# Kernel optimization log

Measured on AMD Instinct MI355X. Metric: run time of the kernel, lower is better.

## Reference

```python
import jax, jax.numpy as jnp
import numpy as np

E, H, F, T = 8, 2048, 4096, 16384  # experts, hidden, ffn, total tokens


def setup_inputs() -> dict:
    key = jax.random.key(0)
    k1, k2, k3 = jax.random.split(key, 3)
    std = 1.0 / np.sqrt(H)
    x = jax.random.normal(k1, (T, H), dtype=jnp.float32)
    # trunc_normal_(std=std) ~ normal * std for reference purposes
    w_gate_up = jax.random.normal(k2, (E, 2 * F, H), dtype=jnp.float32) * std
    w_down = jax.random.normal(k3, (E, H, F), dtype=jnp.float32) * std
    # tokens are pre-sorted by expert; uniform routing: T//E tokens per expert
    tokens_per_expert = jnp.full((E,), T // E, dtype=jnp.int64)
    return {"x": x, "w_gate_up": w_gate_up, "w_down": w_down,
            "tokens_per_expert": tokens_per_expert}


def reference(x, w_gate_up, w_down, tokens_per_expert):
    # x: [T, H] sorted by expert; uniform tokens_per_expert => grouped GEMM
    # is a batched GEMM over the expert axis (same math as the per-expert
    # sequential fallback: gate_up = xi @ w_gate_up[i].T, etc.).
    e = w_gate_up.shape[0]
    f = w_down.shape[2]
    xe = x.reshape(e, -1, x.shape[-1])                     # [E, T/E, H]
    gate_up = jnp.einsum('eth,efh->etf', xe, w_gate_up)    # [E, T/E, 2F]
    gate, up = gate_up[..., :f], gate_up[..., f:]
    hidden = jax.nn.silu(gate) * up                        # [E, T/E, F]
    out = jnp.einsum('etf,ehf->eth', hidden, w_down)       # [E, T/E, H]
    return out.reshape(x.shape)
```

## Files before the change

### kernel.cpp

```cpp
#include <hip/hip_runtime.h>
#include <stdint.h>

typedef unsigned short u16;
typedef unsigned int u32;
typedef short bf16x8 __attribute__((ext_vector_type(8)));
typedef float f32x4 __attribute__((ext_vector_type(4)));

#define E_ 8
#define H_ 2048
#define F_ 4096
#define T_ 16384
#define TE_ 2048

#define WAITV(n) asm volatile("s_waitcnt vmcnt(" #n ")" ::: "memory")
#define FENCE asm volatile("" ::: "memory")
#define BAR __builtin_amdgcn_s_barrier()

__device__ __forceinline__ u16 f2bf(float f) {
  u32 u = __builtin_bit_cast(u32, f);
  u32 r = (u + 0x7FFFu + ((u >> 16) & 1u)) >> 16;
  return (u16)r;
}

__device__ __forceinline__ void gload16(const u16* g, u16* l) {
  __builtin_amdgcn_global_load_lds(
      (__attribute__((address_space(1))) void*)g,
      (__attribute__((address_space(3))) void*)l, 16, 0, 0);
}

__device__ __forceinline__ void mfma_b(f32x4& acc, bf16x8 a, bf16x8 b) {
  asm volatile("v_mfma_f32_16x16x32_bf16 %0, %1, %2, %0"
               : "+v"(acc)
               : "v"(a), "v"(b));
}


__global__ __launch_bounds__(256) void cvt_kernel(const float* __restrict__ src,
                                                  u16* __restrict__ dst,
                                                  long n4) {
  long i = (long)blockIdx.x * blockDim.x + threadIdx.x;
  long stride = (long)gridDim.x * blockDim.x;
  const float4* s4 = (const float4*)src;
  uint2* d4 = (uint2*)dst;
  for (; i < n4; i += stride) {
    float4 v = s4[i];
    uint2 o;
    o.x = (u32)f2bf(v.x) | ((u32)f2bf(v.y) << 16);
    o.y = (u32)f2bf(v.z) | ((u32)f2bf(v.w) << 16);
    d4[i] = o;
  }
}


__global__ __launch_bounds__(512) void gemm1_silu(const u16* __restrict__ Xb,
                                                  const u16* __restrict__ Wgu,
                                                  u16* __restrict__ Hid,
                                                  long sX, long sW, long sH) {
  const int z = blockIdx.z;
  Xb += (long)z * sX;
  Wgu += (long)z * sW;
  Hid += (long)z * sH;

  const int bx = blockIdx.x;
  const int by = blockIdx.y;
  const int tid = threadIdx.x;
  const int w = tid >> 6;
  const int lane = tid & 63;
  const int wr = w >> 2, wc = w & 3;

  __shared__ __attribute__((aligned(16))) u16 lds[3 * 24576];

  const int srow = (w << 3) + (lane >> 3);
  const int scol = (((lane & 7) ^ (lane >> 3)) << 3);
  const u16* gA = Xb + (size_t)((by << 7) + srow) * H_ + scol;
  const u16* gBg = Wgu + (size_t)((bx << 7) + srow) * H_ + scol;
  const u16* gBu = gBg + (size_t)F_ * H_;

  auto stage = [&](int t, int buf) {
    u16* L = &lds[buf * 24576];
    const int ko = t << 6;
    const int wb = w << 3;
#pragma unroll
    for (int i = 0; i < 2; ++i) {
      gload16(gA + (size_t)(i * 64) * H_ + ko, &L[((i << 6) + wb) << 6]);
      gload16(gBg + (size_t)(i * 64) * H_ + ko,
              &L[8192 + (((i << 6) + wb) << 6)]);
      gload16(gBu + (size_t)(i * 64) * H_ + ko,
              &L[16384 + (((i << 6) + wb) << 6)]);
    }
  };

  f32x4 accG[4][2] = {};
  f32x4 accU[4][2] = {};
  const int fr = lane & 15, q = lane >> 4, l7 = lane & 7;

  auto comp = [&](int buf) {
    const u16* L = &lds[buf * 24576];
    bf16x8 a[4][2], bg[2][2], bu[2][2];
#pragma unroll
    for (int ni = 0; ni < 2; ++ni)
#pragma unroll
      for (int ks = 0; ks < 2; ++ks) {
        int r = (wc << 5) + (ni << 4) + fr;
        int off = (r << 6) + ((((ks << 2) + q) ^ l7) << 3);
        bg[ni][ks] = *(const bf16x8*)&L[8192 + off];
        bu[ni][ks] = *(const bf16x8*)&L[16384 + off];
      }
#pragma unroll
    for (int mi = 0; mi < 4; ++mi)
#pragma unroll
      for (int ks = 0; ks < 2; ++ks) {
        int r = (wr << 6) + (mi << 4) + fr;
        a[mi][ks] = *(const bf16x8*)&L[(r << 6) + ((((ks << 2) + q) ^ l7) << 3)];
      }
    __builtin_amdgcn_s_setprio(1);
#pragma unroll
    for (int mi = 0; mi < 4; ++mi)
#pragma unroll
      for (int ni = 0; ni < 2; ++ni)
#pragma unroll
        for (int ks = 0; ks < 2; ++ks) {
          mfma_b(accG[mi][ni], a[mi][ks], bg[ni][ks]);
          mfma_b(accU[mi][ni], a[mi][ks], bu[ni][ks]);
        }
    __builtin_amdgcn_s_setprio(0);
  };

  const int NT = H_ / 64;
  stage(0, 0);
  stage(1, 1);
  int b0 = 0, b1 = 1, b2 = 2;
  for (int t = 0; t < NT - 2; ++t) {
    stage(t + 2, b2);
    WAITV(12);
    BAR;
    FENCE;
    comp(b0);
    FENCE;
    BAR;
    int tmp = b0; b0 = b1; b1 = b2; b2 = tmp;
  }
  WAITV(6); BAR; FENCE;
  comp(b0);
  FENCE; BAR;
  WAITV(0); BAR; FENCE;
  comp(b1);

  const int row0 = (by << 7) + (wr << 6) + (q << 2);
  const int col0 = (bx << 7) + (wc << 5) + fr;
#pragma unroll
  for (int mi = 0; mi < 4; ++mi)
#pragma unroll
    for (int ni = 0; ni < 2; ++ni)
#pragma unroll
      for (int j = 0; j < 4; ++j) {
        float g = accG[mi][ni][j];
        float u = accU[mi][ni][j];
        float h = (g / (1.f + __expf(-g))) * u;
        Hid[(size_t)(row0 + (mi << 4) + j) * F_ + col0 + (ni << 4)] = f2bf(h);
      }
}


__global__ __launch_bounds__(512) void gemm2_down(const u16* __restrict__ Hd,
                                                  const u16* __restrict__ Wd,
                                                  float* __restrict__ Out,
                                                  long sH, long sW, long sO) {
  const int z = blockIdx.z;
  Hd += (long)z * sH;
  Wd += (long)z * sW;
  Out += (long)z * sO;

  const int bx = blockIdx.x;
  const int by = blockIdx.y;
  const int tid = threadIdx.x;
  const int w = tid >> 6;
  const int lane = tid & 63;
  const int wr = w >> 1, wc = w & 1;

  __shared__ __attribute__((aligned(16))) u16 lds[3 * 24576];

  const int srow = (w << 3) + (lane >> 3);
  const int scol = (((lane & 7) ^ (lane >> 3)) << 3);
  const u16* gA = Hd + (size_t)((by << 8) + srow) * F_ + scol;
  const u16* gB = Wd + (size_t)((bx << 7) + srow) * F_ + scol;

  auto stage = [&](int t, int buf) {
    u16* L = &lds[buf * 24576];
    const int ko = t << 6;
    const int wb = w << 3;
#pragma unroll
    for (int i = 0; i < 4; ++i)
      gload16(gA + (size_t)(i * 64) * F_ + ko, &L[((i << 6) + wb) << 6]);
#pragma unroll
    for (int i = 0; i < 2; ++i)
      gload16(gB + (size_t)(i * 64) * F_ + ko,
              &L[16384 + (((i << 6) + wb) << 6)]);
  };

  f32x4 acc[4][4] = {};
  const int fr = lane & 15, q = lane >> 4, l7 = lane & 7;

  auto comp = [&](int buf) {
    const u16* L = &lds[buf * 24576];
    bf16x8 a[4][2], b[4][2];
#pragma unroll
    for (int ni = 0; ni < 4; ++ni)
#pragma unroll
      for (int ks = 0; ks < 2; ++ks) {
        int r = (wc << 6) + (ni << 4) + fr;
        b[ni][ks] =
            *(const bf16x8*)&L[16384 + (r << 6) + ((((ks << 2) + q) ^ l7) << 3)];
      }
#pragma unroll
    for (int mi = 0; mi < 4; ++mi)
#pragma unroll
      for (int ks = 0; ks < 2; ++ks) {
        int r = (wr << 6) + (mi << 4) + fr;
        a[mi][ks] = *(const bf16x8*)&L[(r << 6) + ((((ks << 2) + q) ^ l7) << 3)];
      }
    __builtin_amdgcn_s_setprio(1);
#pragma unroll
    for (int mi = 0; mi < 4; ++mi)
#pragma unroll
      for (int ni = 0; ni < 4; ++ni)
#pragma unroll
        for (int ks = 0; ks < 2; ++ks)
          mfma_b(acc[mi][ni], a[mi][ks], b[ni][ks]);
    __builtin_amdgcn_s_setprio(0);
  };

  const int NT = F_ / 64;
  stage(0, 0);
  stage(1, 1);
  int b0 = 0, b1 = 1, b2 = 2;
  for (int t = 0; t < NT - 2; ++t) {
    stage(t + 2, b2);
    WAITV(12);
    BAR;
    FENCE;
    comp(b0);
    FENCE;
    BAR;
    int tmp = b0; b0 = b1; b1 = b2; b2 = tmp;
  }
  WAITV(6); BAR; FENCE;
  comp(b0);
  FENCE; BAR;
  WAITV(0); BAR; FENCE;
  comp(b1);

  const int row0 = (by << 8) + (wr << 6) + (q << 2);
  const int col0 = (bx << 7) + (wc << 6) + fr;
#pragma unroll
  for (int mi = 0; mi < 4; ++mi)
#pragma unroll
    for (int ni = 0; ni < 4; ++ni)
#pragma unroll
      for (int j = 0; j < 4; ++j)
        Out[(size_t)(row0 + (mi << 4) + j) * H_ + col0 + (ni << 4)] =
            acc[mi][ni][j];
}


extern "C" void kernel_launch(void* const* d_in, const int* in_sizes, int n_in,
                              void* d_out, int out_size, void* d_ws,
                              size_t ws_size, hipStream_t stream) {
  (void)in_sizes;
  (void)n_in;
  (void)out_size;
  const float* x = (const float*)d_in[0];
  const float* wgu = (const float*)d_in[1];
  const float* wdn = (const float*)d_in[2];
  float* out = (float*)d_out;
  u16* ws = (u16*)d_ws;

  const size_t xbN = (size_t)T_ * H_;
  const size_t wguN = (size_t)E_ * 2 * F_ * H_;
  const size_t wdnN = (size_t)E_ * H_ * F_;
  const size_t hidN = (size_t)T_ * F_;
  const size_t fullBytes = (xbN + wguN + wdnN + hidN) * 2;

  dim3 cblk(256), gblk(512);

  if (ws_size >= fullBytes) {
    u16* xb = ws;
    u16* wgub = xb + xbN;
    u16* wdnb = wgub + wguN;
    u16* hid = wdnb + wdnN;
    cvt_kernel<<<2048, cblk, 0, stream>>>(x, xb, (long)(xbN / 4));
    cvt_kernel<<<4096, cblk, 0, stream>>>(wgu, wgub, (long)(wguN / 4));
    cvt_kernel<<<4096, cblk, 0, stream>>>(wdn, wdnb, (long)(wdnN / 4));
    gemm1_silu<<<dim3(F_ / 128, TE_ / 128, E_), gblk, 0, stream>>>(
        xb, wgub, hid, (long)TE_ * H_, (long)2 * F_ * H_, (long)TE_ * F_);
    gemm2_down<<<dim3(H_ / 128, TE_ / 256, E_), gblk, 0, stream>>>(
        hid, wdnb, out, (long)TE_ * F_, (long)H_ * F_, (long)TE_ * H_);
  } else {
    u16* xb = ws;
    u16* wgub = xb + (size_t)TE_ * H_;
    u16* wdnb = wgub + (size_t)2 * F_ * H_;
    u16* hid = wdnb + (size_t)H_ * F_;
    for (int e = 0; e < E_; ++e) {
      cvt_kernel<<<1024, cblk, 0, stream>>>(x + (size_t)e * TE_ * H_, xb,
                                            (long)((size_t)TE_ * H_ / 4));
      cvt_kernel<<<2048, cblk, 0, stream>>>(wgu + (size_t)e * 2 * F_ * H_, wgub,
                                            (long)((size_t)2 * F_ * H_ / 4));
      cvt_kernel<<<2048, cblk, 0, stream>>>(wdn + (size_t)e * H_ * F_, wdnb,
                                            (long)((size_t)H_ * F_ / 4));
      gemm1_silu<<<dim3(F_ / 128, TE_ / 128, 1), gblk, 0, stream>>>(xb, wgub,
                                                                    hid, 0, 0,
                                                                    0);
      gemm2_down<<<dim3(H_ / 128, TE_ / 256, 1), gblk, 0, stream>>>(
          hid, wdnb, out + (size_t)e * TE_ * H_, 0, 0, 0);
    }
  }
}
```

Measured before the change: 1.126 ms.

## Rewrite both GEMMs with 256x256 tiles, finer-grained pipelined LDS staging and XCD swizzle

Both GEMM kernels move to 256x256 output tiles per workgroup (gate and up interleaved within the B tile for gemm1). K-chunks are split into half-steps whose loads, LDS reads and MFMA bursts are interleaved with barriers in a double-buffered schedule. Block indices are remapped across chiplets for better L2 locality, and launch bounds ask for 2 waves per SIMD. The goal is higher arithmetic intensity per byte loaded and less stalling on memory. In exchange the kernel holds many more accumulator registers, and the new LDS layout has no XOR swizzle, which may cause bank conflicts.

After: 1.214 ms. +7.8%, slower.

```diff
diff --git a/kernel.cpp b/kernel.cpp
--- a/kernel.cpp
+++ b/kernel.cpp
@@ -13,8 +13,12 @@
 #define TE_ 2048
 
 #define WAITV(n) asm volatile("s_waitcnt vmcnt(" #n ")" ::: "memory")
-#define FENCE asm volatile("" ::: "memory")
-#define BAR __builtin_amdgcn_s_barrier()
+#define BARF                              \
+  do {                                    \
+    asm volatile("" ::: "memory");        \
+    __builtin_amdgcn_s_barrier();         \
+    asm volatile("" ::: "memory");        \
+  } while (0)
 
 __device__ __forceinline__ u16 f2bf(float f) {
   u32 u = __builtin_bit_cast(u32, f);
@@ -52,214 +56,219 @@
 }
 
 
-__global__ __launch_bounds__(512) void gemm1_silu(const u16* __restrict__ Xb,
-                                                  const u16* __restrict__ Wgu,
-                                                  u16* __restrict__ Hid,
-                                                  long sX, long sW, long sH) {
-  const int z = blockIdx.z;
-  Xb += (long)z * sX;
-  Wgu += (long)z * sW;
-  Hid += (long)z * sH;
-
-  const int bx = blockIdx.x;
-  const int by = blockIdx.y;
-  const int tid = threadIdx.x;
-  const int w = tid >> 6;
-  const int lane = tid & 63;
+__global__ __launch_bounds__(512, 2) void gemm1_silu(
+    const u16* __restrict__ Xb, const u16* __restrict__ Wgu,
+    u16* __restrict__ Hid) {
+  const int nx = gridDim.x, ny = gridDim.y;
+  int lin = blockIdx.x + nx * (blockIdx.y + ny * blockIdx.z);
+  const int nwg = nx * ny * gridDim.z;
+  int swz = (lin & 7) * (nwg >> 3) + (lin >> 3);
+  const int bx = swz % nx;
+  int tq = swz / nx;
+  const int by = tq % ny;
+  const int z = tq / ny;
+  Xb += (size_t)z * TE_ * H_;
+  Wgu += (size_t)z * 2 * F_ * H_;
+  Hid += (size_t)z * TE_ * F_;
+
+  const int tid = threadIdx.x, w = tid >> 6, lane = tid & 63;
   const int wr = w >> 2, wc = w & 3;
-
-  __shared__ __attribute__((aligned(16))) u16 lds[3 * 24576];
-
-  const int srow = (w << 3) + (lane >> 3);
-  const int scol = (((lane & 7) ^ (lane >> 3)) << 3);
-  const u16* gA = Xb + (size_t)((by << 7) + srow) * H_ + scol;
-  const u16* gBg = Wgu + (size_t)((bx << 7) + srow) * H_ + scol;
-  const u16* gBu = gBg + (size_t)F_ * H_;
-
-  auto stage = [&](int t, int buf) {
-    u16* L = &lds[buf * 24576];
-    const int ko = t << 6;
-    const int wb = w << 3;
+  const int r15 = lane & 15, g4 = lane >> 4;
+
+  __shared__ __attribute__((aligned(16))) u16 lds[65536];
+
+  const u16* gA = Xb + (size_t)(by * 256 + r15) * H_ + g4 * 8;
+  const u16* gB =
+      Wgu + (size_t)(((w & 1) ? F_ : 0) + bx * 128 + r15) * H_ + g4 * 8;
+
+  auto stA = [&](int t, int kh, int buf) {
 #pragma unroll
     for (int i = 0; i < 2; ++i) {
-      gload16(gA + (size_t)(i * 64) * H_ + ko, &L[((i << 6) + wb) << 6]);
-      gload16(gBg + (size_t)(i * 64) * H_ + ko,
-              &L[8192 + (((i << 6) + wb) << 6)]);
-      gload16(gBu + (size_t)(i * 64) * H_ + ko,
-              &L[16384 + (((i << 6) + wb) << 6)]);
-    }
-  };
-
-  f32x4 accG[4][2] = {};
-  f32x4 accU[4][2] = {};
-  const int fr = lane & 15, q = lane >> 4, l7 = lane & 7;
-
-  auto comp = [&](int buf) {
-    const u16* L = &lds[buf * 24576];
-    bf16x8 a[4][2], bg[2][2], bu[2][2];
-#pragma unroll
-    for (int ni = 0; ni < 2; ++ni)
-#pragma unroll
-      for (int ks = 0; ks < 2; ++ks) {
-        int r = (wc << 5) + (ni << 4) + fr;
-        int off = (r << 6) + ((((ks << 2) + q) ^ l7) << 3);
-        bg[ni][ks] = *(const bf16x8*)&L[8192 + off];
-        bu[ni][ks] = *(const bf16x8*)&L[16384 + off];
+      const int c = i * 8 + w;
+      gload16(gA + (size_t)(c * 16) * H_ + t * 64 + kh * 32,
+              lds + buf * 32768 + kh * 8192 + c * 512);
+    }
+  };
+  auto stB = [&](int t, int kh, int buf) {
+#pragma unroll
+    for (int i = 0; i < 2; ++i) {
+      const int c = i * 8 + w;
+      gload16(gB + (size_t)((i * 4 + (w >> 1)) * 16) * H_ + t * 64 + kh * 32,
+              lds + buf * 32768 + 16384 + kh * 8192 + c * 512);
+    }
+  };
+
+  const u16* ldsA = lds + lane * 8;
+  const u16* ldsB = lds + 16384 + lane * 8;
+
+  f32x4 acc[8][4] = {};
+  bf16x8 a[4], b[4];
+
+  auto dsB = [&](int buf, int kh) {
+#pragma unroll
+    for (int ni = 0; ni < 4; ++ni)
+      b[ni] =
+          *(const bf16x8*)&ldsB[buf * 32768 + kh * 8192 + (wc * 4 + ni) * 512];
+  };
+  auto dsA = [&](int buf, int kh, int mh) {
+#pragma unroll
+    for (int mi = 0; mi < 4; ++mi)
+      a[mi] = *(const bf16x8*)&ldsA[buf * 32768 + kh * 8192 +
+                                    (wr * 8 + mh * 4 + mi) * 512];
+  };
+  auto mm = [&](int mh) {
+    __builtin_amdgcn_s_setprio(1);
+#pragma unroll
+    for (int mi = 0; mi < 4; ++mi)
+#pragma unroll
+      for (int ni = 0; ni < 4; ++ni) mfma_b(acc[mh * 4 + mi][ni], a[mi], b[ni]);
+    __builtin_amdgcn_s_setprio(0);
+  };
+
+  stB(0, 0, 0); stA(0, 0, 0); stB(0, 1, 0); stA(0, 1, 0);
+  stB(1, 0, 1); stA(1, 0, 1); stB(1, 1, 1);
+  WAITV(6);
+  BARF;
+
+  const int NT = H_ / 64;
+  for (int t = 0; t <= NT - 4; t += 2) {
+    dsB(0, 0); dsA(0, 0, 0); stA(t + 1, 1, 1);           BARF; mm(0); BARF;
+    dsA(0, 0, 1);            stB(t + 2, 0, 0);           BARF; mm(1); BARF;
+    dsB(0, 1); dsA(0, 1, 0); stA(t + 2, 0, 0);           BARF; mm(0); BARF;
+    dsA(0, 1, 1);            stB(t + 2, 1, 0); WAITV(6); BARF; mm(1); BARF;
+    dsB(1, 0); dsA(1, 0, 0); stA(t + 2, 1, 0);           BARF; mm(0); BARF;
+    dsA(1, 0, 1);            stB(t + 3, 0, 1);           BARF; mm(1); BARF;
+    dsB(1, 1); dsA(1, 1, 0); stA(t + 3, 0, 1);           BARF; mm(0); BARF;
+    dsA(1, 1, 1);            stB(t + 3, 1, 1); WAITV(6); BARF; mm(1); BARF;
+  }
+  dsB(0, 0); dsA(0, 0, 0); stA(NT - 1, 1, 1); BARF; mm(0); BARF;
+  dsA(0, 0, 1);                               BARF; mm(1); BARF;
+  dsB(0, 1); dsA(0, 1, 0);                    BARF; mm(0); BARF;
+  dsA(0, 1, 1);            WAITV(0);          BARF; mm(1); BARF;
+  dsB(1, 0); dsA(1, 0, 0);                    BARF; mm(0); BARF;
+  dsA(1, 0, 1);                               BARF; mm(1); BARF;
+  dsB(1, 1); dsA(1, 1, 0);                    BARF; mm(0); BARF;
+  dsA(1, 1, 1);                               BARF; mm(1);
+
+  const int row0 = by * 256 + wr * 128 + g4 * 4;
+  const int colb = bx * 128 + wc * 32 + r15;
+#pragma unroll
+  for (int mI = 0; mI < 8; ++mI)
+#pragma unroll
+    for (int k = 0; k < 2; ++k)
+#pragma unroll
+      for (int j = 0; j < 4; ++j) {
+        float g = acc[mI][2 * k][j];
+        float u = acc[mI][2 * k + 1][j];
+        float h = (g / (1.f + __expf(-g))) * u;
+        Hid[(size_t)(row0 + mI * 16 + j) * F_ + colb + k * 16] = f2bf(h);
       }
+}
+
+
+__global__ __launch_bounds__(512, 2) void gemm2_down(
+    const u16* __restrict__ Hd, const u16* __restrict__ Wd,
+    float* __restrict__ Out) {
+  const int nx = gridDim.x, ny = gridDim.y;
+  int lin = blockIdx.x + nx * (blockIdx.y + ny * blockIdx.z);
+  const int nwg = nx * ny * gridDim.z;
+  int swz = (lin & 7) * (nwg >> 3) + (lin >> 3);
+  const int bx = swz % nx;
+  int tq = swz / nx;
+  const int by = tq % ny;
+  const int z = tq / ny;
+  Hd += (size_t)z * TE_ * F_;
+  Wd += (size_t)z * H_ * F_;
+  Out += (size_t)z * TE_ * H_;
+
+  const int tid = threadIdx.x, w = tid >> 6, lane = tid & 63;
+  const int wr = w >> 2, wc = w & 3;
+  const int r15 = lane & 15, g4 = lane >> 4;
+
+  __shared__ __attribute__((aligned(16))) u16 lds[65536];
+
+  const u16* gA = Hd + (size_t)(by * 256 + r15) * F_ + g4 * 8;
+  const u16* gB = Wd + (size_t)(bx * 256 + r15) * F_ + g4 * 8;
+
+  auto stA = [&](int t, int kh, int buf) {
+#pragma unroll
+    for (int i = 0; i < 2; ++i) {
+      const int c = i * 8 + w;
+      gload16(gA + (size_t)(c * 16) * F_ + t * 64 + kh * 32,
+              lds + buf * 32768 + kh * 8192 + c * 512);
+    }
+  };
+  auto stB = [&](int t, int kh, int buf) {
+#pragma unroll
+    for (int i = 0; i < 2; ++i) {
+      const int c = i * 8 + w;
+      gload16(gB + (size_t)(c * 16) * F_ + t * 64 + kh * 32,
+              lds + buf * 32768 + 16384 + kh * 8192 + c * 512);
+    }
+  };
+
+  const u16* ldsA = lds + lane * 8;
+  const u16* ldsB = lds + 16384 + lane * 8;
+
+  f32x4 acc[8][4] = {};
+  bf16x8 a[4], b[4];
+
+  auto dsB = [&](int buf, int kh) {
+#pragma unroll
+    for (int ni = 0; ni < 4; ++ni)
+      b[ni] =
+          *(const bf16x8*)&ldsB[buf * 32768 + kh * 8192 + (wc * 4 + ni) * 512];
+  };
+  auto dsA = [&](int buf, int kh, int mh) {
 #pragma unroll
     for (int mi = 0; mi < 4; ++mi)
-#pragma unroll
-      for (int ks = 0; ks < 2; ++ks) {
-        int r = (wr << 6) + (mi << 4) + fr;
-        a[mi][ks] = *(const bf16x8*)&L[(r << 6) + ((((ks << 2) + q) ^ l7) << 3)];
-      }
+      a[mi] = *(const bf16x8*)&ldsA[buf * 32768 + kh * 8192 +
+                                    (wr * 8 + mh * 4 + mi) * 512];
+  };
+  auto mm = [&](int mh) {
     __builtin_amdgcn_s_setprio(1);
 #pragma unroll
     for (int mi = 0; mi < 4; ++mi)
 #pragma unroll
-      for (int ni = 0; ni < 2; ++ni)
-#pragma unroll
-        for (int ks = 0; ks < 2; ++ks) {
-          mfma_b(accG[mi][ni], a[mi][ks], bg[ni][ks]);
-          mfma_b(accU[mi][ni], a[mi][ks], bu[ni][ks]);
-        }
+      for (int ni = 0; ni < 4; ++ni) mfma_b(acc[mh * 4 + mi][ni], a[mi], b[ni]);
     __builtin_amdgcn_s_setprio(0);
   };
 
-  const int NT = H_ / 64;
-  stage(0, 0);
-  stage(1, 1);
-  int b0 = 0, b1 = 1, b2 = 2;
-  for (int t = 0; t < NT - 2; ++t) {
-    stage(t + 2, b2);
-    WAITV(12);
-    BAR;
-    FENCE;
-    comp(b0);
-    FENCE;
-    BAR;
-    int tmp = b0; b0 = b1; b1 = b2; b2 = tmp;
+  stB(0, 0, 0); stA(0, 0, 0); stB(0, 1, 0); stA(0, 1, 0);
+  stB(1, 0, 1); stA(1, 0, 1); stB(1, 1, 1);
+  WAITV(6);
+  BARF;
+
+  const int NT = F_ / 64;
+  for (int t = 0; t <= NT - 4; t += 2) {
+    dsB(0, 0); dsA(0, 0, 0); stA(t + 1, 1, 1);           BARF; mm(0); BARF;
+    dsA(0, 0, 1);            stB(t + 2, 0, 0);           BARF; mm(1); BARF;
+    dsB(0, 1); dsA(0, 1, 0); stA(t + 2, 0, 0);           BARF; mm(0); BARF;
+    dsA(0, 1, 1);            stB(t + 2, 1, 0); WAITV(6); BARF; mm(1); BARF;
+    dsB(1, 0); dsA(1, 0, 0); stA(t + 2, 1, 0);           BARF; mm(0); BARF;
+    dsA(1, 0, 1);            stB(t + 3, 0, 1);           BARF; mm(1); BARF;
+    dsB(1, 1); dsA(1, 1, 0); stA(t + 3, 0, 1);           BARF; mm(0); BARF;
+    dsA(1, 1, 1);            stB(t + 3, 1, 1); WAITV(6); BARF; mm(1); BARF;
   }
-  WAITV(6); BAR; FENCE;
-  comp(b0);
-  FENCE; BAR;
-  WAITV(0); BAR; FENCE;
-  comp(b1);
-
-  const int row0 = (by << 7) + (wr << 6) + (q << 2);
-  const int col0 = (bx << 7) + (wc << 5) + fr;
-#pragma unroll
-  for (int mi = 0; mi < 4; ++mi)
-#pragma unroll
-    for (int ni = 0; ni < 2; ++ni)
-#pragma unroll
-      for (int j = 0; j < 4; ++j) {
-        float g = accG[mi][ni][j];
-        float u = accU[mi][ni][j];
-        float h = (g / (1.f + __expf(-g))) * u;
-        Hid[(size_t)(row0 + (mi << 4) + j) * F_ + col0 + (ni << 4)] = f2bf(h);
-      }
-}
-
-
-__global__ __launch_bounds__(512) void gemm2_down(const u16* __restrict__ Hd,
-                                                  const u16* __restrict__ Wd,
-                                                  float* __restrict__ Out,
-                                                  long sH, long sW, long sO) {
-  const int z = blockIdx.z;
-  Hd += (long)z * sH;
-  Wd += (long)z * sW;
-  Out += (long)z * sO;
-
-  const int bx = blockIdx.x;
-  const int by = blockIdx.y;
-  const int tid = threadIdx.x;
-  const int w = tid >> 6;
-  const int lane = tid & 63;
-  const int wr = w >> 1, wc = w & 1;
-
-  __shared__ __attribute__((aligned(16))) u16 lds[3 * 24576];
-
-  const int srow = (w << 3) + (lane >> 3);
-  const int scol = (((lane & 7) ^ (lane >> 3)) << 3);
-  const u16* gA = Hd + (size_t)((by << 8) + srow) * F_ + scol;
-  const u16* gB = Wd + (size_t)((bx << 7) + srow) * F_ + scol;
-
-  auto stage = [&](int t, int buf) {
-    u16* L = &lds[buf * 24576];
-    const int ko = t << 6;
-    const int wb = w << 3;
-#pragma unroll
-    for (int i = 0; i < 4; ++i)
-      gload16(gA + (size_t)(i * 64) * F_ + ko, &L[((i << 6) + wb) << 6]);
-#pragma unroll
-    for (int i = 0; i < 2; ++i)
-      gload16(gB + (size_t)(i * 64) * F_ + ko,
-              &L[16384 + (((i << 6) + wb) << 6)]);
-  };
-
-  f32x4 acc[4][4] = {};
-  const int fr = lane & 15, q = lane >> 4, l7 = lane & 7;
-
-  auto comp = [&](int buf) {
-    const u16* L = &lds[buf * 24576];
-    bf16x8 a[4][2], b[4][2];
+  dsB(0, 0); dsA(0, 0, 0); stA(NT - 1, 1, 1); BARF; mm(0); BARF;
+  dsA(0, 0, 1);                               BARF; mm(1); BARF;
+  dsB(0, 1); dsA(0, 1, 0);                    BARF; mm(0); BARF;
+  dsA(0, 1, 1);            WAITV(0);          BARF; mm(1); BARF;
+  dsB(1, 0); dsA(1, 0, 0);                    BARF; mm(0); BARF;
+  dsA(1, 0, 1);                               BARF; mm(1); BARF;
+  dsB(1, 1); dsA(1, 1, 0);                    BARF; mm(0); BARF;
+  dsA(1, 1, 1);                               BARF; mm(1);
+
+  const int row0 = by * 256 + wr * 128 + g4 * 4;
+  const int col0 = bx * 256 + wc * 64 + r15;
+#pragma unroll
+  for (int mI = 0; mI < 8; ++mI)
 #pragma unroll
     for (int ni = 0; ni < 4; ++ni)
 #pragma unroll
-      for (int ks = 0; ks < 2; ++ks) {
-        int r = (wc << 6) + (ni << 4) + fr;
-        b[ni][ks] =
-            *(const bf16x8*)&L[16384 + (r << 6) + ((((ks << 2) + q) ^ l7) << 3)];
-      }
-#pragma unroll
-    for (int mi = 0; mi < 4; ++mi)
-#pragma unroll
-      for (int ks = 0; ks < 2; ++ks) {
-        int r = (wr << 6) + (mi << 4) + fr;
-        a[mi][ks] = *(const bf16x8*)&L[(r << 6) + ((((ks << 2) + q) ^ l7) << 3)];
-      }
-    __builtin_amdgcn_s_setprio(1);
-#pragma unroll
-    for (int mi = 0; mi < 4; ++mi)
-#pragma unroll
-      for (int ni = 0; ni < 4; ++ni)
-#pragma unroll
-        for (int ks = 0; ks < 2; ++ks)
-          mfma_b(acc[mi][ni], a[mi][ks], b[ni][ks]);
-    __builtin_amdgcn_s_setprio(0);
-  };
-
-  const int NT = F_ / 64;
-  stage(0, 0);
-  stage(1, 1);
-  int b0 = 0, b1 = 1, b2 = 2;
-  for (int t = 0; t < NT - 2; ++t) {
-    stage(t + 2, b2);
-    WAITV(12);
-    BAR;
-    FENCE;
-    comp(b0);
-    FENCE;
-    BAR;
-    int tmp = b0; b0 = b1; b1 = b2; b2 = tmp;
-  }
-  WAITV(6); BAR; FENCE;
-  comp(b0);
-  FENCE; BAR;
-  WAITV(0); BAR; FENCE;
-  comp(b1);
-
-  const int row0 = (by << 8) + (wr << 6) + (q << 2);
-  const int col0 = (bx << 7) + (wc << 6) + fr;
-#pragma unroll
-  for (int mi = 0; mi < 4; ++mi)
-#pragma unroll
-    for (int ni = 0; ni < 4; ++ni)
-#pragma unroll
       for (int j = 0; j < 4; ++j)
-        Out[(size_t)(row0 + (mi << 4) + j) * H_ + col0 + (ni << 4)] =
-            acc[mi][ni][j];
+        Out[(size_t)(row0 + mI * 16 + j) * H_ + col0 + ni * 16] =
+            acc[mI][ni][j];
 }
 
 
@@ -291,10 +300,10 @@
     cvt_kernel<<<2048, cblk, 0, stream>>>(x, xb, (long)(xbN / 4));
     cvt_kernel<<<4096, cblk, 0, stream>>>(wgu, wgub, (long)(wguN / 4));
     cvt_kernel<<<4096, cblk, 0, stream>>>(wdn, wdnb, (long)(wdnN / 4));
-    gemm1_silu<<<dim3(F_ / 128, TE_ / 128, E_), gblk, 0, stream>>>(
-        xb, wgub, hid, (long)TE_ * H_, (long)2 * F_ * H_, (long)TE_ * F_);
-    gemm2_down<<<dim3(H_ / 128, TE_ / 256, E_), gblk, 0, stream>>>(
-        hid, wdnb, out, (long)TE_ * F_, (long)H_ * F_, (long)TE_ * H_);
+    gemm1_silu<<<dim3(F_ / 128, TE_ / 256, E_), gblk, 0, stream>>>(xb, wgub,
+                                                                   hid);
+    gemm2_down<<<dim3(H_ / 256, TE_ / 256, E_), gblk, 0, stream>>>(hid, wdnb,
+                                                                   out);
   } else {
     u16* xb = ws;
     u16* wgub = xb + (size_t)TE_ * H_;
@@ -307,11 +316,10 @@
                                             (long)((size_t)2 * F_ * H_ / 4));
       cvt_kernel<<<2048, cblk, 0, stream>>>(wdn + (size_t)e * H_ * F_, wdnb,
                                             (long)((size_t)H_ * F_ / 4));
-      gemm1_silu<<<dim3(F_ / 128, TE_ / 128, 1), gblk, 0, stream>>>(xb, wgub,
-                                                                    hid, 0, 0,
-                                                                    0);
-      gemm2_down<<<dim3(H_ / 128, TE_ / 256, 1), gblk, 0, stream>>>(
-          hid, wdnb, out + (size_t)e * TE_ * H_, 0, 0, 0);
+      gemm1_silu<<<dim3(F_ / 128, TE_ / 256, 1), gblk, 0, stream>>>(xb, wgub,
+                                                                    hid);
+      gemm2_down<<<dim3(H_ / 256, TE_ / 256, 1), gblk, 0, stream>>>(
+          hid, wdnb, out + (size_t)e * TE_ * H_);
     }
   }
 }
```

## Enlarge gemm1 tile to 256 rows with fragment-ordered LDS and double buffering

Applied to the files above, without the earlier changes.

The gate/up GEMM tile grows from 128x128 to 256 token rows by 128 ffn columns, with each wave holding a 64x64 output for both gate and up. Staged data is written to LDS in MFMA-fragment order with no XOR swizzle, and the three-buffer ring becomes a two-buffer ring where the next stage is issued after the post-compute barrier. The aim is more reuse per LDS byte and fewer global loads per flop, at the cost of twice the accumulator registers per wave and less overlap between loads and compute. The barrier/fence macros are merged, which also touches gemm2.

New measurement: 1.186 ms. +5.3%, slower.

```diff
diff --git a/kernel.cpp b/kernel.cpp
--- a/kernel.cpp
+++ b/kernel.cpp
@@ -13,8 +13,12 @@
 #define TE_ 2048
 
 #define WAITV(n) asm volatile("s_waitcnt vmcnt(" #n ")" ::: "memory")
-#define FENCE asm volatile("" ::: "memory")
-#define BAR __builtin_amdgcn_s_barrier()
+#define BARF                       \
+  do {                             \
+    asm volatile("" ::: "memory"); \
+    __builtin_amdgcn_s_barrier();  \
+    asm volatile("" ::: "memory"); \
+  } while (0)
 
 __device__ __forceinline__ u16 f2bf(float f) {
   u32 u = __builtin_bit_cast(u32, f);
@@ -52,112 +56,104 @@
 }
 
 
-__global__ __launch_bounds__(512) void gemm1_silu(const u16* __restrict__ Xb,
-                                                  const u16* __restrict__ Wgu,
-                                                  u16* __restrict__ Hid,
-                                                  long sX, long sW, long sH) {
-  const int z = blockIdx.z;
-  Xb += (long)z * sX;
-  Wgu += (long)z * sW;
-  Hid += (long)z * sH;
-
+__global__ __launch_bounds__(512, 2) void gemm1_silu(
+    const u16* __restrict__ Xb, const u16* __restrict__ Wgu,
+    u16* __restrict__ Hid) {
   const int bx = blockIdx.x;
   const int by = blockIdx.y;
-  const int tid = threadIdx.x;
-  const int w = tid >> 6;
-  const int lane = tid & 63;
-  const int wr = w >> 2, wc = w & 3;
-
-  __shared__ __attribute__((aligned(16))) u16 lds[3 * 24576];
-
-  const int srow = (w << 3) + (lane >> 3);
-  const int scol = (((lane & 7) ^ (lane >> 3)) << 3);
-  const u16* gA = Xb + (size_t)((by << 7) + srow) * H_ + scol;
-  const u16* gBg = Wgu + (size_t)((bx << 7) + srow) * H_ + scol;
-  const u16* gBu = gBg + (size_t)F_ * H_;
+  const int z = blockIdx.z;
+  Xb += (size_t)z * TE_ * H_;
+  Wgu += (size_t)z * 2 * F_ * H_;
+  Hid += (size_t)z * TE_ * F_;
+
+  const int tid = threadIdx.x, w = tid >> 6, lane = tid & 63;
+  const int rq = w >> 1, ch = w & 1;
+  const int r15 = lane & 15, g4 = lane >> 4;
+
+  __shared__ __attribute__((aligned(16))) u16 lds[65536];
+
+  const u16* gA = Xb + (size_t)(by * 256 + r15) * H_ + g4 * 8;
+  const u16* gBg = Wgu + (size_t)(bx * 128 + r15) * H_ + g4 * 8;
+  const u16* gBu = Wgu + (size_t)(F_ + bx * 128 + r15) * H_ + g4 * 8;
 
   auto stage = [&](int t, int buf) {
-    u16* L = &lds[buf * 24576];
-    const int ko = t << 6;
-    const int wb = w << 3;
+    u16* L = lds + buf * 32768;
+    const int kb = t * 64;
+#pragma unroll
+    for (int i = 0; i < 4; ++i) {
+      const int c = i * 8 + w, rg = c >> 1, ks = c & 1;
+      gload16(gA + (size_t)(rg * 16) * H_ + kb + ks * 32,
+              L + c * 512 + lane * 8);
+    }
 #pragma unroll
     for (int i = 0; i < 2; ++i) {
-      gload16(gA + (size_t)(i * 64) * H_ + ko, &L[((i << 6) + wb) << 6]);
-      gload16(gBg + (size_t)(i * 64) * H_ + ko,
-              &L[8192 + (((i << 6) + wb) << 6)]);
-      gload16(gBu + (size_t)(i * 64) * H_ + ko,
-              &L[16384 + (((i << 6) + wb) << 6)]);
+      const int c = i * 8 + w, rg = c >> 1, ks = c & 1;
+      gload16(gBg + (size_t)(rg * 16) * H_ + kb + ks * 32,
+              L + 16384 + c * 512 + lane * 8);
+    }
+#pragma unroll
+    for (int i = 2; i < 4; ++i) {
+      const int c = i * 8 + w, rg = (c >> 1) - 8, ks = c & 1;
+      gload16(gBu + (size_t)(rg * 16) * H_ + kb + ks * 32,
+              L + 16384 + c * 512 + lane * 8);
     }
   };
 
-  f32x4 accG[4][2] = {};
-  f32x4 accU[4][2] = {};
-  const int fr = lane & 15, q = lane >> 4, l7 = lane & 7;
+  f32x4 accG[4][4] = {};
+  f32x4 accU[4][4] = {};
 
   auto comp = [&](int buf) {
-    const u16* L = &lds[buf * 24576];
-    bf16x8 a[4][2], bg[2][2], bu[2][2];
-#pragma unroll
-    for (int ni = 0; ni < 2; ++ni)
-#pragma unroll
-      for (int ks = 0; ks < 2; ++ks) {
-        int r = (wc << 5) + (ni << 4) + fr;
-        int off = (r << 6) + ((((ks << 2) + q) ^ l7) << 3);
-        bg[ni][ks] = *(const bf16x8*)&L[8192 + off];
-        bu[ni][ks] = *(const bf16x8*)&L[16384 + off];
+    const u16* LA = lds + buf * 32768 + lane * 8;
+    const u16* LB = LA + 16384;
+#pragma unroll
+    for (int ks = 0; ks < 2; ++ks) {
+      bf16x8 a[4], bg[4], bu[4];
+#pragma unroll
+      for (int mi = 0; mi < 4; ++mi)
+        a[mi] = *(const bf16x8*)&LA[((rq * 4 + mi) * 2 + ks) * 512];
+#pragma unroll
+      for (int ni = 0; ni < 4; ++ni) {
+        bg[ni] = *(const bf16x8*)&LB[((ch * 4 + ni) * 2 + ks) * 512];
+        bu[ni] = *(const bf16x8*)&LB[((8 + ch * 4 + ni) * 2 + ks) * 512];
       }
-#pragma unroll
-    for (int mi = 0; mi < 4; ++mi)
-#pragma unroll
-      for (int ks = 0; ks < 2; ++ks) {
-        int r = (wr << 6) + (mi << 4) + fr;
-        a[mi][ks] = *(const bf16x8*)&L[(r << 6) + ((((ks << 2) + q) ^ l7) << 3)];
-      }
-    __builtin_amdgcn_s_setprio(1);
-#pragma unroll
-    for (int mi = 0; mi < 4; ++mi)
-#pragma unroll
-      for (int ni = 0; ni < 2; ++ni)
-#pragma unroll
-        for (int ks = 0; ks < 2; ++ks) {
-          mfma_b(accG[mi][ni], a[mi][ks], bg[ni][ks]);
-          mfma_b(accU[mi][ni], a[mi][ks], bu[ni][ks]);
+      __builtin_amdgcn_s_setprio(1);
+#pragma unroll
+      for (int mi = 0; mi < 4; ++mi)
+#pragma unroll
+        for (int ni = 0; ni < 4; ++ni) {
+          mfma_b(accG[mi][ni], a[mi], bg[ni]);
+          mfma_b(accU[mi][ni], a[mi], bu[ni]);
         }
-    __builtin_amdgcn_s_setprio(0);
+      __builtin_amdgcn_s_setprio(0);
+    }
   };
 
   const int NT = H_ / 64;
   stage(0, 0);
   stage(1, 1);
-  int b0 = 0, b1 = 1, b2 = 2;
-  for (int t = 0; t < NT - 2; ++t) {
-    stage(t + 2, b2);
-    WAITV(12);
-    BAR;
-    FENCE;
-    comp(b0);
-    FENCE;
-    BAR;
-    int tmp = b0; b0 = b1; b1 = b2; b2 = tmp;
+  for (int t = 0; t < NT - 1; ++t) {
+    WAITV(8);
+    BARF;
+    comp(t & 1);
+    BARF;
+    if (t + 2 < NT) stage(t + 2, t & 1);
   }
-  WAITV(6); BAR; FENCE;
-  comp(b0);
-  FENCE; BAR;
-  WAITV(0); BAR; FENCE;
-  comp(b1);
-
-  const int row0 = (by << 7) + (wr << 6) + (q << 2);
-  const int col0 = (bx << 7) + (wc << 5) + fr;
+  WAITV(0);
+  BARF;
+  comp((NT - 1) & 1);
+
+  const int row0 = by * 256 + rq * 64 + g4 * 4;
+  const int col0 = bx * 128 + ch * 64 + r15;
 #pragma unroll
   for (int mi = 0; mi < 4; ++mi)
 #pragma unroll
-    for (int ni = 0; ni < 2; ++ni)
+    for (int ni = 0; ni < 4; ++ni)
 #pragma unroll
       for (int j = 0; j < 4; ++j) {
         float g = accG[mi][ni][j];
         float u = accU[mi][ni][j];
         float h = (g / (1.f + __expf(-g))) * u;
-        Hid[(size_t)(row0 + (mi << 4) + j) * F_ + col0 + (ni << 4)] = f2bf(h);
+        Hid[(size_t)(row0 + mi * 16 + j) * F_ + col0 + ni * 16] = f2bf(h);
       }
 }
 
@@ -237,17 +233,15 @@
   for (int t = 0; t < NT - 2; ++t) {
     stage(t + 2, b2);
     WAITV(12);
-    BAR;
-    FENCE;
+    BARF;
     comp(b0);
-    FENCE;
-    BAR;
+    BARF;
     int tmp = b0; b0 = b1; b1 = b2; b2 = tmp;
   }
-  WAITV(6); BAR; FENCE;
+  WAITV(6); BARF;
   comp(b0);
-  FENCE; BAR;
-  WAITV(0); BAR; FENCE;
+  BARF;
+  WAITV(0); BARF;
   comp(b1);
 
   const int row0 = (by << 8) + (wr << 6) + (q << 2);
@@ -291,8 +285,8 @@
     cvt_kernel<<<2048, cblk, 0, stream>>>(x, xb, (long)(xbN / 4));
     cvt_kernel<<<4096, cblk, 0, stream>>>(wgu, wgub, (long)(wguN / 4));
     cvt_kernel<<<4096, cblk, 0, stream>>>(wdn, wdnb, (long)(wdnN / 4));
-    gemm1_silu<<<dim3(F_ / 128, TE_ / 128, E_), gblk, 0, stream>>>(
-        xb, wgub, hid, (long)TE_ * H_, (long)2 * F_ * H_, (long)TE_ * F_);
+    gemm1_silu<<<dim3(F_ / 128, TE_ / 256, E_), gblk, 0, stream>>>(xb, wgub,
+                                                                   hid);
     gemm2_down<<<dim3(H_ / 128, TE_ / 256, E_), gblk, 0, stream>>>(
         hid, wdnb, out, (long)TE_ * F_, (long)H_ * F_, (long)TE_ * H_);
   } else {
@@ -307,9 +301,8 @@
                                             (long)((size_t)2 * F_ * H_ / 4));
       cvt_kernel<<<2048, cblk, 0, stream>>>(wdn + (size_t)e * H_ * F_, wdnb,
                                             (long)((size_t)H_ * F_ / 4));
-      gemm1_silu<<<dim3(F_ / 128, TE_ / 128, 1), gblk, 0, stream>>>(xb, wgub,
-                                                                    hid, 0, 0,
-                                                                    0);
+      gemm1_silu<<<dim3(F_ / 128, TE_ / 256, 1), gblk, 0, stream>>>(xb, wgub,
+                                                                    hid);
       gemm2_down<<<dim3(H_ / 128, TE_ / 256, 1), gblk, 0, stream>>>(
           hid, wdnb, out + (size_t)e * TE_ * H_, 0, 0, 0);
     }
```

## Switch GEMMs to 32x32x16 MFMA tiles and merge conversion kernels

Applied to the files above, without the earlier changes.

Both GEMM kernels replace the 16x16x32 bf16 MFMA with the 32x32x16 variant. Each wave now issues fewer, larger matrix instructions with fewer LDS fragment loads per k-step, and the epilogue index mapping is rewritten for the 32x32 accumulator layout. The three fp32-to-bf16 conversion launches are merged into one kernel that writes a contiguous workspace, removing launch overhead at the cost of per-element branching. The compute loop now interleaves LDS loads with MFMAs per k-substep, which may expose LDS latency.

Result: slower. 1.175 ms (+4.3%).

```diff
diff --git a/kernel.cpp b/kernel.cpp
--- a/kernel.cpp
+++ b/kernel.cpp
@@ -4,7 +4,7 @@
 typedef unsigned short u16;
 typedef unsigned int u32;
 typedef short bf16x8 __attribute__((ext_vector_type(8)));
-typedef float f32x4 __attribute__((ext_vector_type(4)));
+typedef float f32x16 __attribute__((ext_vector_type(16)));
 
 #define E_ 8
 #define H_ 2048
@@ -13,8 +13,12 @@
 #define TE_ 2048
 
 #define WAITV(n) asm volatile("s_waitcnt vmcnt(" #n ")" ::: "memory")
-#define FENCE asm volatile("" ::: "memory")
-#define BAR __builtin_amdgcn_s_barrier()
+#define BARF                       \
+  do {                             \
+    asm volatile("" ::: "memory"); \
+    __builtin_amdgcn_s_barrier();  \
+    asm volatile("" ::: "memory"); \
+  } while (0)
 
 __device__ __forceinline__ u16 f2bf(float f) {
   u32 u = __builtin_bit_cast(u32, f);
@@ -28,22 +32,35 @@
       (__attribute__((address_space(3))) void*)l, 16, 0, 0);
 }
 
-__device__ __forceinline__ void mfma_b(f32x4& acc, bf16x8 a, bf16x8 b) {
-  asm volatile("v_mfma_f32_16x16x32_bf16 %0, %1, %2, %0"
+__device__ __forceinline__ void mfma32(f32x16& acc, bf16x8 a, bf16x8 b) {
+  asm volatile("v_mfma_f32_32x32x16_bf16 %0, %1, %2, %0"
                : "+v"(acc)
                : "v"(a), "v"(b));
 }
 
 
-__global__ __launch_bounds__(256) void cvt_kernel(const float* __restrict__ src,
-                                                  u16* __restrict__ dst,
-                                                  long n4) {
+__global__ __launch_bounds__(256) void cvt3_kernel(
+    const float* __restrict__ s0, const float* __restrict__ s1,
+    const float* __restrict__ s2, u16* __restrict__ dst, long n0, long n1,
+    long n2) {
   long i = (long)blockIdx.x * blockDim.x + threadIdx.x;
   long stride = (long)gridDim.x * blockDim.x;
-  const float4* s4 = (const float4*)src;
+  const long ntot = n0 + n1 + n2;
   uint2* d4 = (uint2*)dst;
-  for (; i < n4; i += stride) {
-    float4 v = s4[i];
+  for (; i < ntot; i += stride) {
+    const float4* s4;
+    long j;
+    if (i < n0) {
+      s4 = (const float4*)s0;
+      j = i;
+    } else if (i < n0 + n1) {
+      s4 = (const float4*)s1;
+      j = i - n0;
+    } else {
+      s4 = (const float4*)s2;
+      j = i - n0 - n1;
+    }
+    float4 v = s4[j];
     uint2 o;
     o.x = (u32)f2bf(v.x) | ((u32)f2bf(v.y) << 16);
     o.y = (u32)f2bf(v.z) | ((u32)f2bf(v.w) << 16);
@@ -67,6 +84,7 @@
   const int w = tid >> 6;
   const int lane = tid & 63;
   const int wr = w >> 2, wc = w & 3;
+  const int l31 = lane & 31, q2 = lane >> 5, l7 = lane & 7;
 
   __shared__ __attribute__((aligned(16))) u16 lds[3 * 24576];
 
@@ -90,40 +108,25 @@
     }
   };
 
-  f32x4 accG[4][2] = {};
-  f32x4 accU[4][2] = {};
-  const int fr = lane & 15, q = lane >> 4, l7 = lane & 7;
+  f32x16 accG[2] = {};
+  f32x16 accU[2] = {};
 
   auto comp = [&](int buf) {
     const u16* L = &lds[buf * 24576];
-    bf16x8 a[4][2], bg[2][2], bu[2][2];
-#pragma unroll
-    for (int ni = 0; ni < 2; ++ni)
-#pragma unroll
-      for (int ks = 0; ks < 2; ++ks) {
-        int r = (wc << 5) + (ni << 4) + fr;
-        int off = (r << 6) + ((((ks << 2) + q) ^ l7) << 3);
-        bg[ni][ks] = *(const bf16x8*)&L[8192 + off];
-        bu[ni][ks] = *(const bf16x8*)&L[16384 + off];
-      }
-#pragma unroll
-    for (int mi = 0; mi < 4; ++mi)
-#pragma unroll
-      for (int ks = 0; ks < 2; ++ks) {
-        int r = (wr << 6) + (mi << 4) + fr;
-        a[mi][ks] = *(const bf16x8*)&L[(r << 6) + ((((ks << 2) + q) ^ l7) << 3)];
-      }
-    __builtin_amdgcn_s_setprio(1);
-#pragma unroll
-    for (int mi = 0; mi < 4; ++mi)
-#pragma unroll
-      for (int ni = 0; ni < 2; ++ni)
-#pragma unroll
-        for (int ks = 0; ks < 2; ++ks) {
-          mfma_b(accG[mi][ni], a[mi][ks], bg[ni][ks]);
-          mfma_b(accU[mi][ni], a[mi][ks], bu[ni][ks]);
-        }
-    __builtin_amdgcn_s_setprio(0);
+#pragma unroll
+    for (int ks = 0; ks < 4; ++ks) {
+      const int seg = (((ks << 1) + q2) ^ l7) << 3;
+      bf16x8 a0 = *(const bf16x8*)&L[((wr << 6) + l31) * 64 + seg];
+      bf16x8 a1 = *(const bf16x8*)&L[((wr << 6) + 32 + l31) * 64 + seg];
+      bf16x8 bg = *(const bf16x8*)&L[8192 + ((wc << 5) + l31) * 64 + seg];
+      bf16x8 bu = *(const bf16x8*)&L[16384 + ((wc << 5) + l31) * 64 + seg];
+      __builtin_amdgcn_s_setprio(1);
+      mfma32(accG[0], a0, bg);
+      mfma32(accU[0], a0, bu);
+      mfma32(accG[1], a1, bg);
+      mfma32(accU[1], a1, bu);
+      __builtin_amdgcn_s_setprio(0);
+    }
   };
 
   const int NT = H_ / 64;
@@ -133,32 +136,29 @@
   for (int t = 0; t < NT - 2; ++t) {
     stage(t + 2, b2);
     WAITV(12);
-    BAR;
-    FENCE;
+    BARF;
     comp(b0);
-    FENCE;
-    BAR;
+    BARF;
     int tmp = b0; b0 = b1; b1 = b2; b2 = tmp;
   }
-  WAITV(6); BAR; FENCE;
+  WAITV(6); BARF;
   comp(b0);
-  FENCE; BAR;
-  WAITV(0); BAR; FENCE;
+  BARF;
+  WAITV(0); BARF;
   comp(b1);
 
-  const int row0 = (by << 7) + (wr << 6) + (q << 2);
-  const int col0 = (bx << 7) + (wc << 5) + fr;
-#pragma unroll
-  for (int mi = 0; mi < 4; ++mi)
-#pragma unroll
-    for (int ni = 0; ni < 2; ++ni)
-#pragma unroll
-      for (int j = 0; j < 4; ++j) {
-        float g = accG[mi][ni][j];
-        float u = accU[mi][ni][j];
-        float h = (g / (1.f + __expf(-g))) * u;
-        Hid[(size_t)(row0 + (mi << 4) + j) * F_ + col0 + (ni << 4)] = f2bf(h);
-      }
+  const int row0 = (by << 7) + (wr << 6);
+  const int col = (bx << 7) + (wc << 5) + l31;
+#pragma unroll
+  for (int mi = 0; mi < 2; ++mi)
+#pragma unroll
+    for (int r = 0; r < 16; ++r) {
+      const int trow = row0 + mi * 32 + (r & 3) + ((r >> 2) << 3) + (q2 << 2);
+      float g = accG[mi][r];
+      float u = accU[mi][r];
+      float h = (g / (1.f + __expf(-g))) * u;
+      Hid[(size_t)trow * F_ + col] = f2bf(h);
+    }
 }
 
 
@@ -177,6 +177,7 @@
   const int w = tid >> 6;
   const int lane = tid & 63;
   const int wr = w >> 1, wc = w & 1;
+  const int l31 = lane & 31, q2 = lane >> 5, l7 = lane & 7;
 
   __shared__ __attribute__((aligned(16))) u16 lds[3 * 24576];
 
@@ -198,36 +199,24 @@
               &L[16384 + (((i << 6) + wb) << 6)]);
   };
 
-  f32x4 acc[4][4] = {};
-  const int fr = lane & 15, q = lane >> 4, l7 = lane & 7;
+  f32x16 acc[2][2] = {};
 
   auto comp = [&](int buf) {
     const u16* L = &lds[buf * 24576];
-    bf16x8 a[4][2], b[4][2];
-#pragma unroll
-    for (int ni = 0; ni < 4; ++ni)
-#pragma unroll
-      for (int ks = 0; ks < 2; ++ks) {
-        int r = (wc << 6) + (ni << 4) + fr;
-        b[ni][ks] =
-            *(const bf16x8*)&L[16384 + (r << 6) + ((((ks << 2) + q) ^ l7) << 3)];
-      }
-#pragma unroll
-    for (int mi = 0; mi < 4; ++mi)
-#pragma unroll
-      for (int ks = 0; ks < 2; ++ks) {
-        int r = (wr << 6) + (mi << 4) + fr;
-        a[mi][ks] = *(const bf16x8*)&L[(r << 6) + ((((ks << 2) + q) ^ l7) << 3)];
-      }
-    __builtin_amdgcn_s_setprio(1);
-#pragma unroll
-    for (int mi = 0; mi < 4; ++mi)
-#pragma unroll
-      for (int ni = 0; ni < 4; ++ni)
-#pragma unroll
-        for (int ks = 0; ks < 2; ++ks)
-          mfma_b(acc[mi][ni], a[mi][ks], b[ni][ks]);
-    __builtin_amdgcn_s_setprio(0);
+#pragma unroll
+    for (int ks = 0; ks < 4; ++ks) {
+      const int seg = (((ks << 1) + q2) ^ l7) << 3;
+      bf16x8 a0 = *(const bf16x8*)&L[((wr << 6) + l31) * 64 + seg];
+      bf16x8 a1 = *(const bf16x8*)&L[((wr << 6) + 32 + l31) * 64 + seg];
+      bf16x8 b0 = *(const bf16x8*)&L[16384 + ((wc << 6) + l31) * 64 + seg];
+      bf16x8 b1 = *(const bf16x8*)&L[16384 + ((wc << 6) + 32 + l31) * 64 + seg];
+      __builtin_amdgcn_s_setprio(1);
+      mfma32(acc[0][0], a0, b0);
+      mfma32(acc[0][1], a0, b1);
+      mfma32(acc[1][0], a1, b0);
+      mfma32(acc[1][1], a1, b1);
+      __builtin_amdgcn_s_setprio(0);
+    }
   };
 
   const int NT = F_ / 64;
@@ -237,29 +226,30 @@
   for (int t = 0; t < NT - 2; ++t) {
     stage(t + 2, b2);
     WAITV(12);
-    BAR;
-    FENCE;
+    BARF;
     comp(b0);
-    FENCE;
-    BAR;
+    BARF;
     int tmp = b0; b0 = b1; b1 = b2; b2 = tmp;
   }
-  WAITV(6); BAR; FENCE;
+  WAITV(6); BARF;
   comp(b0);
-  FENCE; BAR;
-  WAITV(0); BAR; FENCE;
+  BARF;
+  WAITV(0); BARF;
   comp(b1);
 
-  const int row0 = (by << 8) + (wr << 6) + (q << 2);
-  const int col0 = (bx << 7) + (wc << 6) + fr;
-#pragma unroll
-  for (int mi = 0; mi < 4; ++mi)
-#pragma unroll
-    for (int ni = 0; ni < 4; ++ni)
-#pragma unroll
-      for (int j = 0; j < 4; ++j)
-        Out[(size_t)(row0 + (mi << 4) + j) * H_ + col0 + (ni << 4)] =
-            acc[mi][ni][j];
+  const int row0 = (by << 8) + (wr << 6);
+  const int col0 = (bx << 7) + (wc << 6);
+#pragma unroll
+  for (int mi = 0; mi < 2; ++mi)
+#pragma unroll
+    for (int ni = 0; ni < 2; ++ni)
+#pragma unroll
+      for (int r = 0; r < 16; ++r) {
+        const int trow =
+            row0 + mi * 32 + (r & 3) + ((r >> 2) << 3) + (q2 << 2);
+        const int tcol = col0 + ni * 32 + l31;
+        Out[(size_t)trow * H_ + tcol] = acc[mi][ni][r];
+      }
 }
 
 
@@ -288,9 +278,8 @@
     u16* wgub = xb + xbN;
     u16* wdnb = wgub + wguN;
     u16* hid = wdnb + wdnN;
-    cvt_kernel<<<2048, cblk, 0, stream>>>(x, xb, (long)(xbN / 4));
-    cvt_kernel<<<4096, cblk, 0, stream>>>(wgu, wgub, (long)(wguN / 4));
-    cvt_kernel<<<4096, cblk, 0, stream>>>(wdn, wdnb, (long)(wdnN / 4));
+    cvt3_kernel<<<4096, cblk, 0, stream>>>(x, wgu, wdn, ws, (long)(xbN / 4),
+                                           (long)(wguN / 4), (long)(wdnN / 4));
     gemm1_silu<<<dim3(F_ / 128, TE_ / 128, E_), gblk, 0, stream>>>(
         xb, wgub, hid, (long)TE_ * H_, (long)2 * F_ * H_, (long)TE_ * F_);
     gemm2_down<<<dim3(H_ / 128, TE_ / 256, E_), gblk, 0, stream>>>(
@@ -301,12 +290,10 @@
     u16* wdnb = wgub + (size_t)2 * F_ * H_;
     u16* hid = wdnb + (size_t)H_ * F_;
     for (int e = 0; e < E_; ++e) {
-      cvt_kernel<<<1024, cblk, 0, stream>>>(x + (size_t)e * TE_ * H_, xb,
-                                            (long)((size_t)TE_ * H_ / 4));
-      cvt_kernel<<<2048, cblk, 0, stream>>>(wgu + (size_t)e * 2 * F_ * H_, wgub,
-                                            (long)((size_t)2 * F_ * H_ / 4));
-      cvt_kernel<<<2048, cblk, 0, stream>>>(wdn + (size_t)e * H_ * F_, wdnb,
-                                            (long)((size_t)H_ * F_ / 4));
+      cvt3_kernel<<<2048, cblk, 0, stream>>>(
+          x + (size_t)e * TE_ * H_, wgu + (size_t)e * 2 * F_ * H_,
+          wdn + (size_t)e * H_ * F_, ws, (long)((size_t)TE_ * H_ / 4),
+          (long)((size_t)2 * F_ * H_ / 4), (long)((size_t)H_ * F_ / 4));
       gemm1_silu<<<dim3(F_ / 128, TE_ / 128, 1), gblk, 0, stream>>>(xb, wgub,
                                                                     hid, 0, 0,
                                                                     0);
```
